# Kernel tuning notes

Measured on AMD Instinct MI355X. Metric: run time of the kernel, lower is better.

Reference implementation:

```python
import jax, jax.numpy as jnp
import numpy as np

MAX_LENGTH = 256
WIDTH = 4


def _attention_matrix(a, b):
    # a, b: (B, M, D) with M = max_length + width - 1
    # euclidean match score: 1 / (1 + ||a_i - b_j||_2)
    sq = (
        jnp.sum(a * a, axis=-1)[:, :, None]
        + jnp.sum(b * b, axis=-1)[:, None, :]
        - 2.0 * jnp.einsum('bid,bjd->bij', a, b)
    )
    dist = jnp.sqrt(jnp.maximum(sq, 0.0))
    return 1.0 / (1.0 + dist)  # (B, M, M)


def reference(x1, x2):
    # x1, x2: (B, 1, M, D), M = MAX_LENGTH + WIDTH - 1
    a = x1[:, 0]  # (B, M, D)
    b = x2[:, 0]
    A = _attention_matrix(a, b)  # (B, M, M), A[b,i,j] = score(a_i, b_j)
    # row_sum over dim i of A[:,:,k] weights x1 column k; col analogously for x2.
    w_a = jnp.sum(A, axis=1)  # (B, M): sum_i A[i, k]
    w_b = jnp.sum(A, axis=2)  # (B, M): sum_j A[k, j]
    y1 = w_a[:, :, None] * a  # (B, M, D)
    y2 = w_b[:, :, None] * b
    # sliding-window sum of width WIDTH: w[j] = sum_{k=j}^{j+WIDTH-1} y[k]
    w1 = sum(y1[:, d:d + MAX_LENGTH, :] for d in range(WIDTH))
    w2 = sum(y2[:, d:d + MAX_LENGTH, :] for d in range(WIDTH))
    return (w1[:, None], w2[:, None])  # (B, 1, MAX_LENGTH, D) each


def setup_inputs() -> dict:
    key = jax.random.key(0)
    k1, k2 = jax.random.split(key)
    B, M, D = 128, MAX_LENGTH + WIDTH - 1, 512
    x1 = jax.random.normal(k1, (B, 1, M, D), dtype=jnp.float32)
    x2 = jax.random.normal(k2, (B, 1, M, D), dtype=jnp.float32)
    return {"x1": x1, "x2": x2}
```

## Files before the change

### kernel.cpp

```cpp
#include <hip/hip_runtime.h>

#define BATCH 128
#define M 259
#define D 512
#define T 256
#define NM (BATCH * M)
#define OUTHALF (BATCH * T * D)

typedef __bf16 bf16;
typedef __bf16 bf16x4 __attribute__((ext_vector_type(4)));
typedef __bf16 bf16x8 __attribute__((ext_vector_type(8)));
typedef float f32x4 __attribute__((ext_vector_type(4)));


__global__ void k_norms(const float* __restrict__ x1, const float* __restrict__ x2,
                        float* __restrict__ ws) {
    int wave = blockIdx.x * 4 + (threadIdx.x >> 6);
    int lane = threadIdx.x & 63;
    if (wave >= NM) return;
    const float4* p1 = (const float4*)(x1 + (size_t)wave * D);
    const float4* p2 = (const float4*)(x2 + (size_t)wave * D);
    float s1 = 0.f, s2 = 0.f;
#pragma unroll
    for (int q = 0; q < 2; ++q) {
        float4 v = p1[lane + q * 64];
        s1 += v.x * v.x + v.y * v.y + v.z * v.z + v.w * v.w;
        float4 w = p2[lane + q * 64];
        s2 += w.x * w.x + w.y * w.y + w.z * w.z + w.w * w.w;
    }
#pragma unroll
    for (int off = 32; off > 0; off >>= 1) {
        s1 += __shfl_xor(s1, off);
        s2 += __shfl_xor(s2, off);
    }
    if (lane == 0) {
        ws[wave]          = s1;
        ws[NM + wave]     = s2;
        ws[2 * NM + wave] = 0.f;
        ws[3 * NM + wave] = 0.f;
    }
}

#define BT 96
#define BK 64
#define NTL 3

__launch_bounds__(256)
__global__ void k_pairs(const float* __restrict__ x1, const float* __restrict__ x2,
                        float* __restrict__ ws) {
    __shared__ __align__(16) bf16 As[2][BT * BK];
    __shared__ __align__(16) bf16 Bs[2][BT * BK];

    int s   = blockIdx.x;
    int bid = (s & 7) * 144 + (s >> 3);
    int b   = bid / 9;
    int ti  = (bid % 9) / 3;
    int tj  = bid % 3;
    int i0  = ti * BT, j0 = tj * BT;

    int t    = threadIdx.x;
    int lane = t & 63;
    int w    = t >> 6;
    int wm   = w >> 1, wn = w & 1;
    int iw   = i0 + wm * 48;
    int jw   = j0 + wn * 48;

    const float* Ab = x1 + (size_t)b * M * D;
    const float* Bb = x2 + (size_t)b * M * D;

    const float* pa[6];
    const float* pb[6];
    int c4 = (t & 15) * 4;
#pragma unroll
    for (int p = 0; p < 6; ++p) {
        int ra = min(i0 + p * 16 + (t >> 4), M - 1);
        int rb = min(j0 + p * 16 + (t >> 4), M - 1);
        pa[p] = Ab + (size_t)ra * D + c4;
        pb[p] = Bb + (size_t)rb * D + c4;
    }
    int wslot   = (t & 15) >> 1;
    int wwithin = (t & 1) * 4;
    int wr_off[6];
#pragma unroll
    for (int p = 0; p < 6; ++p) {
        int row = p * 16 + (t >> 4);
        wr_off[p] = row * BK + ((wslot ^ (row & 7)) << 3) + wwithin;
    }

    int a_off[3][2], b_off[3][2];
#pragma unroll
    for (int fm = 0; fm < 3; ++fm) {
        int rowa = wm * 48 + fm * 16 + (lane & 15);
        int rowb = wn * 48 + fm * 16 + (lane & 15);
#pragma unroll
        for (int kk = 0; kk < 2; ++kk) {
            int slot = kk * 4 + (lane >> 4);
            a_off[fm][kk] = rowa * BK + ((slot ^ (rowa & 7)) << 3);
            b_off[fm][kk] = rowb * BK + ((slot ^ (rowb & 7)) << 3);
        }
    }

    f32x4 acc[3][3];
#pragma unroll
    for (int fm = 0; fm < 3; ++fm)
#pragma unroll
        for (int fn = 0; fn < 3; ++fn) acc[fm][fn] = (f32x4)0.f;

    float4 va[6], vb[6];
#pragma unroll
    for (int p = 0; p < 6; ++p) {
        va[p] = *(const float4*)(pa[p]);
        vb[p] = *(const float4*)(pb[p]);
    }
#pragma unroll
    for (int p = 0; p < 6; ++p) {
        bf16x4 ca = { (bf16)va[p].x, (bf16)va[p].y, (bf16)va[p].z, (bf16)va[p].w };
        bf16x4 cb = { (bf16)vb[p].x, (bf16)vb[p].y, (bf16)vb[p].z, (bf16)vb[p].w };
        *(bf16x4*)&As[0][wr_off[p]] = ca;
        *(bf16x4*)&Bs[0][wr_off[p]] = cb;
    }
    __syncthreads();
#pragma unroll
    for (int p = 0; p < 6; ++p) {
        va[p] = *(const float4*)(pa[p] + BK);
        vb[p] = *(const float4*)(pb[p] + BK);
    }

    for (int k0 = 0; k0 < D; k0 += BK) {
        int cur = (k0 >> 6) & 1;
#pragma unroll
        for (int kk = 0; kk < 2; ++kk) {
            bf16x8 af[3], bfr[3];
#pragma unroll
            for (int fm = 0; fm < 3; ++fm) af[fm]  = *(const bf16x8*)&As[cur][a_off[fm][kk]];
#pragma unroll
            for (int fn = 0; fn < 3; ++fn) bfr[fn] = *(const bf16x8*)&Bs[cur][b_off[fn][kk]];
#pragma unroll
            for (int fm = 0; fm < 3; ++fm)
#pragma unroll
                for (int fn = 0; fn < 3; ++fn)
                    acc[fm][fn] = __builtin_amdgcn_mfma_f32_16x16x32_bf16(
                        af[fm], bfr[fn], acc[fm][fn], 0, 0, 0);
        }
        if (k0 + BK < D) {
#pragma unroll
            for (int p = 0; p < 6; ++p) {
                bf16x4 ca = { (bf16)va[p].x, (bf16)va[p].y, (bf16)va[p].z, (bf16)va[p].w };
                bf16x4 cb = { (bf16)vb[p].x, (bf16)vb[p].y, (bf16)vb[p].z, (bf16)vb[p].w };
                *(bf16x4*)&As[cur ^ 1][wr_off[p]] = ca;
                *(bf16x4*)&Bs[cur ^ 1][wr_off[p]] = cb;
            }
            __syncthreads();
            if (k0 + 2 * BK < D) {
#pragma unroll
                for (int p = 0; p < 6; ++p) {
                    va[p] = *(const float4*)(pa[p] + k0 + 2 * BK);
                    vb[p] = *(const float4*)(pb[p] + k0 + 2 * BK);
                }
            }
        }
    }

    int b_off_w = b * M;
    float na_[3][4], nb_[3];
#pragma unroll
    for (int fm = 0; fm < 3; ++fm)
#pragma unroll
        for (int r = 0; r < 4; ++r) {
            int i = iw + fm * 16 + (lane >> 4) * 4 + r;
            na_[fm][r] = (i < M) ? ws[b_off_w + i] : 0.f;
        }
#pragma unroll
    for (int fn = 0; fn < 3; ++fn) {
        int j = jw + fn * 16 + (lane & 15);
        nb_[fn] = (j < M) ? ws[NM + b_off_w + j] : 0.f;
    }

    float rs[3][4];
    float cs[3];
#pragma unroll
    for (int fm = 0; fm < 3; ++fm)
#pragma unroll
        for (int r = 0; r < 4; ++r) rs[fm][r] = 0.f;
#pragma unroll
    for (int fn = 0; fn < 3; ++fn) cs[fn] = 0.f;

#pragma unroll
    for (int fm = 0; fm < 3; ++fm) {
#pragma unroll
        for (int fn = 0; fn < 3; ++fn) {
#pragma unroll
            for (int r = 0; r < 4; ++r) {
                int i = iw + fm * 16 + (lane >> 4) * 4 + r;
                int j = jw + fn * 16 + (lane & 15);
                float av = 0.f;
                if (i < M && j < M) {
                    float sq   = na_[fm][r] + nb_[fn] - 2.f * acc[fm][fn][r];
                    float dist = sqrtf(fmaxf(sq, 0.f));
                    av = 1.f / (1.f + dist);
                }
                rs[fm][r] += av;
                cs[fn]    += av;
            }
        }
    }

#pragma unroll
    for (int fm = 0; fm < 3; ++fm)
#pragma unroll
        for (int r = 0; r < 4; ++r) {
            float v = rs[fm][r];
            v += __shfl_xor(v, 1); v += __shfl_xor(v, 2);
            v += __shfl_xor(v, 4); v += __shfl_xor(v, 8);
            int i = iw + fm * 16 + (lane >> 4) * 4 + r;
            if ((lane & 15) == 0 && i < M) atomicAdd(&ws[3 * NM + b_off_w + i], v);
        }
#pragma unroll
    for (int fn = 0; fn < 3; ++fn) {
        float v = cs[fn];
        v += __shfl_xor(v, 16); v += __shfl_xor(v, 32);
        int j = jw + fn * 16 + (lane & 15);
        if ((lane >> 4) == 0 && j < M) atomicAdd(&ws[2 * NM + b_off_w + j], v);
    }
}

__global__ void k_out(const float* __restrict__ x1, const float* __restrict__ x2,
                      const float* __restrict__ ws, float* __restrict__ out) {
    int bid   = blockIdx.x;
    int which = bid & 1;
    int tc    = (bid >> 1) & 7;
    int b     = bid >> 4;
    int d4    = threadIdx.x << 2;
    const float* src  = which ? x2 : x1;
    const float* wgt  = ws + (which ? 3 * NM : 2 * NM) + b * M;
    const float* rows = src + (size_t)b * M * D + d4;
    float* o = out + (size_t)which * OUTHALF + ((size_t)b * T + tc * 32) * D + d4;
    int t0 = tc * 32;
    float4 v0 = *(const float4*)(rows + (size_t)(t0 + 0) * D);
    float4 v1 = *(const float4*)(rows + (size_t)(t0 + 1) * D);
    float4 v2 = *(const float4*)(rows + (size_t)(t0 + 2) * D);
    float s0 = wgt[t0 + 0], s1 = wgt[t0 + 1], s2 = wgt[t0 + 2];
#pragma unroll 4
    for (int tt = 0; tt < 32; ++tt) {
        float4 v3 = *(const float4*)(rows + (size_t)(t0 + tt + 3) * D);
        float s3  = wgt[t0 + tt + 3];
        float4 r;
        r.x = s0 * v0.x + s1 * v1.x + s2 * v2.x + s3 * v3.x;
        r.y = s0 * v0.y + s1 * v1.y + s2 * v2.y + s3 * v3.y;
        r.z = s0 * v0.z + s1 * v1.z + s2 * v2.z + s3 * v3.z;
        r.w = s0 * v0.w + s1 * v1.w + s2 * v2.w + s3 * v3.w;
        *(float4*)(o + (size_t)tt * D) = r;
        v0 = v1; v1 = v2; v2 = v3;
        s0 = s1; s1 = s2; s2 = s3;
    }
}

extern "C" void kernel_launch(void* const* d_in, const int* in_sizes, int n_in,
                              void* d_out, int out_size, void* d_ws, size_t ws_size,
                              hipStream_t stream) {
    const float* x1 = (const float*)d_in[0];
    const float* x2 = (const float*)d_in[1];
    float* out = (float*)d_out;
    float* ws  = (float*)d_ws;

    k_norms<<<NM / 4, 256, 0, stream>>>(x1, x2, ws);
    k_pairs<<<BATCH * NTL * NTL, 256, 0, stream>>>(x1, x2, ws);
    k_out<<<BATCH * 16, 128, 0, stream>>>(x1, x2, ws, out);
}
```

Baseline: 117.3 us.

## Pre-convert inputs to bf16 and stream GEMM tiles via global_load_lds

The norm kernel now also writes bf16 copies of both inputs into workspace. The pair kernel then loads those copies straight into LDS with the global_load_lds builtin, using an XOR-swizzled layout, instead of loading fp32, converting and storing through registers. The intent is to halve GEMM global traffic and remove conversion work from the main loop, at the cost of an extra bf16 write and re-read pass. A single-buffered fp32 fallback runs when the workspace is too small.

After: 135.1 us. +15.2%, slower.

```diff
diff --git a/kernel.cpp b/kernel.cpp
--- a/kernel.cpp
+++ b/kernel.cpp
@@ -13,31 +13,42 @@
 typedef float f32x4 __attribute__((ext_vector_type(4)));
 
 
-__global__ void k_norms(const float* __restrict__ x1, const float* __restrict__ x2,
-                        float* __restrict__ ws) {
-    int wave = blockIdx.x * 4 + (threadIdx.x >> 6);
+__device__ __forceinline__ void gload16(const bf16* g, bf16* l) {
+    __builtin_amdgcn_global_load_lds(
+        (const __attribute__((address_space(1))) void*)g,
+        (__attribute__((address_space(3))) void*)l, 16, 0, 0);
+}
+
+__global__ void k_prep(const float* __restrict__ x1, const float* __restrict__ x2,
+                       float* __restrict__ ws, bf16* __restrict__ abf,
+                       bf16* __restrict__ bbf) {
+    int row  = blockIdx.x * 4 + (threadIdx.x >> 6);
     int lane = threadIdx.x & 63;
-    if (wave >= NM) return;
-    const float4* p1 = (const float4*)(x1 + (size_t)wave * D);
-    const float4* p2 = (const float4*)(x2 + (size_t)wave * D);
-    float s1 = 0.f, s2 = 0.f;
-#pragma unroll
-    for (int q = 0; q < 2; ++q) {
-        float4 v = p1[lane + q * 64];
-        s1 += v.x * v.x + v.y * v.y + v.z * v.z + v.w * v.w;
-        float4 w = p2[lane + q * 64];
-        s2 += w.x * w.x + w.y * w.y + w.z * w.z + w.w * w.w;
-    }
+    if (row >= NM) return;
+    const float4* p1 = (const float4*)(x1 + (size_t)row * D);
+    const float4* p2 = (const float4*)(x2 + (size_t)row * D);
+    float4 a0 = p1[lane], a1 = p1[lane + 64];
+    float4 b0 = p2[lane], b1 = p2[lane + 64];
+    float s1 = a0.x * a0.x + a0.y * a0.y + a0.z * a0.z + a0.w * a0.w
+             + a1.x * a1.x + a1.y * a1.y + a1.z * a1.z + a1.w * a1.w;
+    float s2 = b0.x * b0.x + b0.y * b0.y + b0.z * b0.z + b0.w * b0.w
+             + b1.x * b1.x + b1.y * b1.y + b1.z * b1.z + b1.w * b1.w;
+    bf16* ar = abf + (size_t)row * D;
+    bf16* br = bbf + (size_t)row * D;
+    *(bf16x4*)(ar + 4 * lane)       = bf16x4{ (bf16)a0.x, (bf16)a0.y, (bf16)a0.z, (bf16)a0.w };
+    *(bf16x4*)(ar + 256 + 4 * lane) = bf16x4{ (bf16)a1.x, (bf16)a1.y, (bf16)a1.z, (bf16)a1.w };
+    *(bf16x4*)(br + 4 * lane)       = bf16x4{ (bf16)b0.x, (bf16)b0.y, (bf16)b0.z, (bf16)b0.w };
+    *(bf16x4*)(br + 256 + 4 * lane) = bf16x4{ (bf16)b1.x, (bf16)b1.y, (bf16)b1.z, (bf16)b1.w };
 #pragma unroll
     for (int off = 32; off > 0; off >>= 1) {
         s1 += __shfl_xor(s1, off);
         s2 += __shfl_xor(s2, off);
     }
     if (lane == 0) {
-        ws[wave]          = s1;
-        ws[NM + wave]     = s2;
-        ws[2 * NM + wave] = 0.f;
-        ws[3 * NM + wave] = 0.f;
+        ws[row]          = s1;
+        ws[NM + row]     = s2;
+        ws[2 * NM + row] = 0.f;
+        ws[3 * NM + row] = 0.f;
     }
 }
 
@@ -46,8 +57,8 @@
 #define NTL 3
 
 __launch_bounds__(256)
-__global__ void k_pairs(const float* __restrict__ x1, const float* __restrict__ x2,
-                        float* __restrict__ ws) {
+__global__ void k_pairs_bf(const bf16* __restrict__ gA0, const bf16* __restrict__ gB0,
+                           float* __restrict__ ws) {
     __shared__ __align__(16) bf16 As[2][BT * BK];
     __shared__ __align__(16) bf16 Bs[2][BT * BK];
 
@@ -65,26 +76,17 @@
     int iw   = i0 + wm * 48;
     int jw   = j0 + wn * 48;
 
-    const float* Ab = x1 + (size_t)b * M * D;
-    const float* Bb = x2 + (size_t)b * M * D;
-
-    const float* pa[6];
-    const float* pb[6];
-    int c4 = (t & 15) * 4;
-#pragma unroll
-    for (int p = 0; p < 6; ++p) {
-        int ra = min(i0 + p * 16 + (t >> 4), M - 1);
-        int rb = min(j0 + p * 16 + (t >> 4), M - 1);
-        pa[p] = Ab + (size_t)ra * D + c4;
-        pb[p] = Bb + (size_t)rb * D + c4;
-    }
-    int wslot   = (t & 15) >> 1;
-    int wwithin = (t & 1) * 4;
-    int wr_off[6];
-#pragma unroll
-    for (int p = 0; p < 6; ++p) {
-        int row = p * 16 + (t >> 4);
-        wr_off[p] = row * BK + ((wslot ^ (row & 7)) << 3) + wwithin;
+    const bf16* gA = gA0 + (size_t)b * M * D;
+    const bf16* gB = gB0 + (size_t)b * M * D;
+
+    int wrow0 = w * 24;
+    int lrow  = lane >> 3;
+    int sl    = (lane & 7) ^ lrow;
+    int rA[3], rB[3];
+#pragma unroll
+    for (int i = 0; i < 3; ++i) {
+        rA[i] = min(i0 + wrow0 + 8 * i + lrow, M - 1);
+        rB[i] = min(j0 + wrow0 + 8 * i + lrow, M - 1);
     }
 
     int a_off[3][2], b_off[3][2];
@@ -106,28 +108,23 @@
 #pragma unroll
         for (int fn = 0; fn < 3; ++fn) acc[fm][fn] = (f32x4)0.f;
 
-    float4 va[6], vb[6];
-#pragma unroll
-    for (int p = 0; p < 6; ++p) {
-        va[p] = *(const float4*)(pa[p]);
-        vb[p] = *(const float4*)(pb[p]);
-    }
-#pragma unroll
-    for (int p = 0; p < 6; ++p) {
-        bf16x4 ca = { (bf16)va[p].x, (bf16)va[p].y, (bf16)va[p].z, (bf16)va[p].w };
-        bf16x4 cb = { (bf16)vb[p].x, (bf16)vb[p].y, (bf16)vb[p].z, (bf16)vb[p].w };
-        *(bf16x4*)&As[0][wr_off[p]] = ca;
-        *(bf16x4*)&Bs[0][wr_off[p]] = cb;
+#pragma unroll
+    for (int i = 0; i < 3; ++i) {
+        gload16(gA + (size_t)rA[i] * D + sl * 8, &As[0][(wrow0 + 8 * i) * BK]);
+        gload16(gB + (size_t)rB[i] * D + sl * 8, &Bs[0][(wrow0 + 8 * i) * BK]);
     }
     __syncthreads();
-#pragma unroll
-    for (int p = 0; p < 6; ++p) {
-        va[p] = *(const float4*)(pa[p] + BK);
-        vb[p] = *(const float4*)(pb[p] + BK);
-    }
-
-    for (int k0 = 0; k0 < D; k0 += BK) {
-        int cur = (k0 >> 6) & 1;
+
+    for (int t8 = 0; t8 < 8; ++t8) {
+        int cur = t8 & 1;
+        if (t8 + 1 < 8) {
+            int k0 = (t8 + 1) * BK;
+#pragma unroll
+            for (int i = 0; i < 3; ++i) {
+                gload16(gA + (size_t)rA[i] * D + k0 + sl * 8, &As[cur ^ 1][(wrow0 + 8 * i) * BK]);
+                gload16(gB + (size_t)rB[i] * D + k0 + sl * 8, &Bs[cur ^ 1][(wrow0 + 8 * i) * BK]);
+            }
+        }
 #pragma unroll
         for (int kk = 0; kk < 2; ++kk) {
             bf16x8 af[3], bfr[3];
@@ -142,23 +139,7 @@
                     acc[fm][fn] = __builtin_amdgcn_mfma_f32_16x16x32_bf16(
                         af[fm], bfr[fn], acc[fm][fn], 0, 0, 0);
         }
-        if (k0 + BK < D) {
-#pragma unroll
-            for (int p = 0; p < 6; ++p) {
-                bf16x4 ca = { (bf16)va[p].x, (bf16)va[p].y, (bf16)va[p].z, (bf16)va[p].w };
-                bf16x4 cb = { (bf16)vb[p].x, (bf16)vb[p].y, (bf16)vb[p].z, (bf16)vb[p].w };
-                *(bf16x4*)&As[cur ^ 1][wr_off[p]] = ca;
-                *(bf16x4*)&Bs[cur ^ 1][wr_off[p]] = cb;
-            }
-            __syncthreads();
-            if (k0 + 2 * BK < D) {
-#pragma unroll
-                for (int p = 0; p < 6; ++p) {
-                    va[p] = *(const float4*)(pa[p] + k0 + 2 * BK);
-                    vb[p] = *(const float4*)(pb[p] + k0 + 2 * BK);
-                }
-            }
-        }
+        __syncthreads();
     }
 
     int b_off_w = b * M;
@@ -176,8 +157,7 @@
         nb_[fn] = (j < M) ? ws[NM + b_off_w + j] : 0.f;
     }
 
-    float rs[3][4];
-    float cs[3];
+    float rs[3][4], cs[3];
 #pragma unroll
     for (int fm = 0; fm < 3; ++fm)
 #pragma unroll
@@ -205,6 +185,167 @@
         }
     }
 
+#pragma unroll
+    for (int fm = 0; fm < 3; ++fm)
+#pragma unroll
+        for (int r = 0; r < 4; ++r) {
+            float v = rs[fm][r];
+            v += __shfl_xor(v, 1); v += __shfl_xor(v, 2);
+            v += __shfl_xor(v, 4); v += __shfl_xor(v, 8);
+            int i = iw + fm * 16 + (lane >> 4) * 4 + r;
+            if ((lane & 15) == 0 && i < M) atomicAdd(&ws[3 * NM + b_off_w + i], v);
+        }
+#pragma unroll
+    for (int fn = 0; fn < 3; ++fn) {
+        float v = cs[fn];
+        v += __shfl_xor(v, 16); v += __shfl_xor(v, 32);
+        int j = jw + fn * 16 + (lane & 15);
+        if ((lane >> 4) == 0 && j < M) atomicAdd(&ws[2 * NM + b_off_w + j], v);
+    }
+}
+
+__global__ void k_norms(const float* __restrict__ x1, const float* __restrict__ x2,
+                        float* __restrict__ ws) {
+    int row  = blockIdx.x * 4 + (threadIdx.x >> 6);
+    int lane = threadIdx.x & 63;
+    if (row >= NM) return;
+    const float4* p1 = (const float4*)(x1 + (size_t)row * D);
+    const float4* p2 = (const float4*)(x2 + (size_t)row * D);
+    float s1 = 0.f, s2 = 0.f;
+#pragma unroll
+    for (int q = 0; q < 2; ++q) {
+        float4 v = p1[lane + q * 64];
+        s1 += v.x * v.x + v.y * v.y + v.z * v.z + v.w * v.w;
+        float4 u = p2[lane + q * 64];
+        s2 += u.x * u.x + u.y * u.y + u.z * u.z + u.w * u.w;
+    }
+#pragma unroll
+    for (int off = 32; off > 0; off >>= 1) {
+        s1 += __shfl_xor(s1, off);
+        s2 += __shfl_xor(s2, off);
+    }
+    if (lane == 0) {
+        ws[row] = s1; ws[NM + row] = s2;
+        ws[2 * NM + row] = 0.f; ws[3 * NM + row] = 0.f;
+    }
+}
+
+__launch_bounds__(256)
+__global__ void k_pairs_fb(const float* __restrict__ x1, const float* __restrict__ x2,
+                           float* __restrict__ ws) {
+    __shared__ __align__(16) bf16 As[BT * BK];
+    __shared__ __align__(16) bf16 Bs[BT * BK];
+    int s   = blockIdx.x;
+    int bid = (s & 7) * 144 + (s >> 3);
+    int b   = bid / 9;
+    int ti  = (bid % 9) / 3;
+    int tj  = bid % 3;
+    int i0  = ti * BT, j0 = tj * BT;
+    int t    = threadIdx.x;
+    int lane = t & 63;
+    int w    = t >> 6;
+    int wm   = w >> 1, wn = w & 1;
+    int iw   = i0 + wm * 48, jw = j0 + wn * 48;
+    const float* Ab = x1 + (size_t)b * M * D;
+    const float* Bb = x2 + (size_t)b * M * D;
+    const float* pa[6]; const float* pb[6];
+    int c4 = (t & 15) * 4;
+#pragma unroll
+    for (int p = 0; p < 6; ++p) {
+        int ra = min(i0 + p * 16 + (t >> 4), M - 1);
+        int rb = min(j0 + p * 16 + (t >> 4), M - 1);
+        pa[p] = Ab + (size_t)ra * D + c4;
+        pb[p] = Bb + (size_t)rb * D + c4;
+    }
+    int wslot = (t & 15) >> 1, wwithin = (t & 1) * 4;
+    int wr_off[6];
+#pragma unroll
+    for (int p = 0; p < 6; ++p) {
+        int row = p * 16 + (t >> 4);
+        wr_off[p] = row * BK + ((wslot ^ (row & 7)) << 3) + wwithin;
+    }
+    int a_off[3][2], b_off[3][2];
+#pragma unroll
+    for (int fm = 0; fm < 3; ++fm) {
+        int rowa = wm * 48 + fm * 16 + (lane & 15);
+        int rowb = wn * 48 + fm * 16 + (lane & 15);
+#pragma unroll
+        for (int kk = 0; kk < 2; ++kk) {
+            int slot = kk * 4 + (lane >> 4);
+            a_off[fm][kk] = rowa * BK + ((slot ^ (rowa & 7)) << 3);
+            b_off[fm][kk] = rowb * BK + ((slot ^ (rowb & 7)) << 3);
+        }
+    }
+    f32x4 acc[3][3];
+#pragma unroll
+    for (int fm = 0; fm < 3; ++fm)
+#pragma unroll
+        for (int fn = 0; fn < 3; ++fn) acc[fm][fn] = (f32x4)0.f;
+    for (int k0 = 0; k0 < D; k0 += BK) {
+        float4 va[6], vb[6];
+#pragma unroll
+        for (int p = 0; p < 6; ++p) {
+            va[p] = *(const float4*)(pa[p] + k0);
+            vb[p] = *(const float4*)(pb[p] + k0);
+        }
+        __syncthreads();
+#pragma unroll
+        for (int p = 0; p < 6; ++p) {
+            *(bf16x4*)&As[wr_off[p]] = bf16x4{ (bf16)va[p].x, (bf16)va[p].y, (bf16)va[p].z, (bf16)va[p].w };
+            *(bf16x4*)&Bs[wr_off[p]] = bf16x4{ (bf16)vb[p].x, (bf16)vb[p].y, (bf16)vb[p].z, (bf16)vb[p].w };
+        }
+        __syncthreads();
+#pragma unroll
+        for (int kk = 0; kk < 2; ++kk) {
+            bf16x8 af[3], bfr[3];
+#pragma unroll
+            for (int fm = 0; fm < 3; ++fm) af[fm]  = *(const bf16x8*)&As[a_off[fm][kk]];
+#pragma unroll
+            for (int fn = 0; fn < 3; ++fn) bfr[fn] = *(const bf16x8*)&Bs[b_off[fn][kk]];
+#pragma unroll
+            for (int fm = 0; fm < 3; ++fm)
+#pragma unroll
+                for (int fn = 0; fn < 3; ++fn)
+                    acc[fm][fn] = __builtin_amdgcn_mfma_f32_16x16x32_bf16(
+                        af[fm], bfr[fn], acc[fm][fn], 0, 0, 0);
+        }
+    }
+    int b_off_w = b * M;
+    float na_[3][4], nb_[3];
+#pragma unroll
+    for (int fm = 0; fm < 3; ++fm)
+#pragma unroll
+        for (int r = 0; r < 4; ++r) {
+            int i = iw + fm * 16 + (lane >> 4) * 4 + r;
+            na_[fm][r] = (i < M) ? ws[b_off_w + i] : 0.f;
+        }
+#pragma unroll
+    for (int fn = 0; fn < 3; ++fn) {
+        int j = jw + fn * 16 + (lane & 15);
+        nb_[fn] = (j < M) ? ws[NM + b_off_w + j] : 0.f;
+    }
+    float rs[3][4], cs[3];
+#pragma unroll
+    for (int fm = 0; fm < 3; ++fm)
+#pragma unroll
+        for (int r = 0; r < 4; ++r) rs[fm][r] = 0.f;
+#pragma unroll
+    for (int fn = 0; fn < 3; ++fn) cs[fn] = 0.f;
+#pragma unroll
+    for (int fm = 0; fm < 3; ++fm)
+#pragma unroll
+        for (int fn = 0; fn < 3; ++fn)
+#pragma unroll
+            for (int r = 0; r < 4; ++r) {
+                int i = iw + fm * 16 + (lane >> 4) * 4 + r;
+                int j = jw + fn * 16 + (lane & 15);
+                float av = 0.f;
+                if (i < M && j < M) {
+                    float sq = na_[fm][r] + nb_[fn] - 2.f * acc[fm][fn][r];
+                    av = 1.f / (1.f + sqrtf(fmaxf(sq, 0.f)));
+                }
+                rs[fm][r] += av; cs[fn] += av;
+            }
 #pragma unroll
     for (int fm = 0; fm < 3; ++fm)
 #pragma unroll
@@ -263,7 +404,15 @@
     float* out = (float*)d_out;
     float* ws  = (float*)d_ws;
 
-    k_norms<<<NM / 4, 256, 0, stream>>>(x1, x2, ws);
-    k_pairs<<<BATCH * NTL * NTL, 256, 0, stream>>>(x1, x2, ws);
+    size_t need = sizeof(float) * 4 * (size_t)NM + sizeof(bf16) * 2 * (size_t)NM * D;
+    if (ws_size >= need) {
+        bf16* abf = (bf16*)(ws + 4 * (size_t)NM);
+        bf16* bbf = abf + (size_t)NM * D;
+        k_prep<<<NM / 4, 256, 0, stream>>>(x1, x2, ws, abf, bbf);
+        k_pairs_bf<<<BATCH * NTL * NTL, 256, 0, stream>>>(abf, bbf, ws);
+    } else {
+        k_norms<<<NM / 4, 256, 0, stream>>>(x1, x2, ws);
+        k_pairs_fb<<<BATCH * NTL * NTL, 256, 0, stream>>>(x1, x2, ws);
+    }
     k_out<<<BATCH * 16, 128, 0, stream>>>(x1, x2, ws, out);
 }
```

## Enlarge pair tile to 144x144 with 9 waves and single-buffered LDS

Applied to the files above, without the earlier changes.

Switches the Gram-matrix kernel from 3x3 tiles of 96 with 4 waves to 2x2 tiles of 144 with 9 waves per block (576 threads). The goal is to cut redundant global loads and fp32-to-bf16 conversions by reusing each loaded row across more of the output tile. It also drops LDS double buffering and register prefetch in favour of a simple load, sync, store, sync loop. That adds two barriers per k-step and exposes global load latency, and the grid shrinks to 512 blocks. The 2x144 tiling also covers rows past M=259, which wastes some compute.

Measured after the change: 119.3 us. About the same (+1.7%).

```diff
diff --git a/kernel.cpp b/kernel.cpp
--- a/kernel.cpp
+++ b/kernel.cpp
@@ -15,18 +15,18 @@
 
 __global__ void k_norms(const float* __restrict__ x1, const float* __restrict__ x2,
                         float* __restrict__ ws) {
-    int wave = blockIdx.x * 4 + (threadIdx.x >> 6);
+    int row  = blockIdx.x * 4 + (threadIdx.x >> 6);
     int lane = threadIdx.x & 63;
-    if (wave >= NM) return;
-    const float4* p1 = (const float4*)(x1 + (size_t)wave * D);
-    const float4* p2 = (const float4*)(x2 + (size_t)wave * D);
+    if (row >= NM) return;
+    const float4* p1 = (const float4*)(x1 + (size_t)row * D);
+    const float4* p2 = (const float4*)(x2 + (size_t)row * D);
     float s1 = 0.f, s2 = 0.f;
 #pragma unroll
     for (int q = 0; q < 2; ++q) {
         float4 v = p1[lane + q * 64];
         s1 += v.x * v.x + v.y * v.y + v.z * v.z + v.w * v.w;
-        float4 w = p2[lane + q * 64];
-        s2 += w.x * w.x + w.y * w.y + w.z * w.z + w.w * w.w;
+        float4 u = p2[lane + q * 64];
+        s2 += u.x * u.x + u.y * u.y + u.z * u.z + u.w * u.w;
     }
 #pragma unroll
     for (int off = 32; off > 0; off >>= 1) {
@@ -34,56 +34,55 @@
         s2 += __shfl_xor(s2, off);
     }
     if (lane == 0) {
-        ws[wave]          = s1;
-        ws[NM + wave]     = s2;
-        ws[2 * NM + wave] = 0.f;
-        ws[3 * NM + wave] = 0.f;
-    }
-}
-
-#define BT 96
+        ws[row]          = s1;
+        ws[NM + row]     = s2;
+        ws[2 * NM + row] = 0.f;
+        ws[3 * NM + row] = 0.f;
+    }
+}
+
+#define BT 144
 #define BK 64
-#define NTL 3
-
-__launch_bounds__(256)
+
 __global__ void k_pairs(const float* __restrict__ x1, const float* __restrict__ x2,
                         float* __restrict__ ws) {
-    __shared__ __align__(16) bf16 As[2][BT * BK];
-    __shared__ __align__(16) bf16 Bs[2][BT * BK];
+    __shared__ __align__(16) bf16 As[BT * BK];
+    __shared__ __align__(16) bf16 Bs[BT * BK];
 
     int s   = blockIdx.x;
-    int bid = (s & 7) * 144 + (s >> 3);
-    int b   = bid / 9;
-    int ti  = (bid % 9) / 3;
-    int tj  = bid % 3;
+    int bid = (s & 7) * 64 + (s >> 3);
+    int b   = bid >> 2;
+    int ti  = (bid >> 1) & 1;
+    int tj  = bid & 1;
     int i0  = ti * BT, j0 = tj * BT;
 
     int t    = threadIdx.x;
     int lane = t & 63;
-    int w    = t >> 6;
-    int wm   = w >> 1, wn = w & 1;
+    int w    = t / 64;
+    int wm   = w / 3, wn = w % 3;
     int iw   = i0 + wm * 48;
     int jw   = j0 + wn * 48;
 
     const float* Ab = x1 + (size_t)b * M * D;
     const float* Bb = x2 + (size_t)b * M * D;
 
-    const float* pa[6];
-    const float* pb[6];
+    const float* pa[4];
+    const float* pb[4];
     int c4 = (t & 15) * 4;
 #pragma unroll
-    for (int p = 0; p < 6; ++p) {
-        int ra = min(i0 + p * 16 + (t >> 4), M - 1);
-        int rb = min(j0 + p * 16 + (t >> 4), M - 1);
+    for (int p = 0; p < 4; ++p) {
+        int row = p * 36 + (t >> 4);
+        int ra = min(i0 + row, M - 1);
+        int rb = min(j0 + row, M - 1);
         pa[p] = Ab + (size_t)ra * D + c4;
         pb[p] = Bb + (size_t)rb * D + c4;
     }
     int wslot   = (t & 15) >> 1;
     int wwithin = (t & 1) * 4;
-    int wr_off[6];
-#pragma unroll
-    for (int p = 0; p < 6; ++p) {
-        int row = p * 16 + (t >> 4);
+    int wr_off[4];
+#pragma unroll
+    for (int p = 0; p < 4; ++p) {
+        int row = p * 36 + (t >> 4);
         wr_off[p] = row * BK + ((wslot ^ (row & 7)) << 3) + wwithin;
     }
 
@@ -106,35 +105,27 @@
 #pragma unroll
         for (int fn = 0; fn < 3; ++fn) acc[fm][fn] = (f32x4)0.f;
 
-    float4 va[6], vb[6];
-#pragma unroll
-    for (int p = 0; p < 6; ++p) {
-        va[p] = *(const float4*)(pa[p]);
-        vb[p] = *(const float4*)(pb[p]);
-    }
-#pragma unroll
-    for (int p = 0; p < 6; ++p) {
-        bf16x4 ca = { (bf16)va[p].x, (bf16)va[p].y, (bf16)va[p].z, (bf16)va[p].w };
-        bf16x4 cb = { (bf16)vb[p].x, (bf16)vb[p].y, (bf16)vb[p].z, (bf16)vb[p].w };
-        *(bf16x4*)&As[0][wr_off[p]] = ca;
-        *(bf16x4*)&Bs[0][wr_off[p]] = cb;
-    }
-    __syncthreads();
-#pragma unroll
-    for (int p = 0; p < 6; ++p) {
-        va[p] = *(const float4*)(pa[p] + BK);
-        vb[p] = *(const float4*)(pb[p] + BK);
-    }
-
     for (int k0 = 0; k0 < D; k0 += BK) {
-        int cur = (k0 >> 6) & 1;
+        float4 va[4], vb[4];
+#pragma unroll
+        for (int p = 0; p < 4; ++p) {
+            va[p] = *(const float4*)(pa[p] + k0);
+            vb[p] = *(const float4*)(pb[p] + k0);
+        }
+        __syncthreads();
+#pragma unroll
+        for (int p = 0; p < 4; ++p) {
+            *(bf16x4*)&As[wr_off[p]] = bf16x4{ (bf16)va[p].x, (bf16)va[p].y, (bf16)va[p].z, (bf16)va[p].w };
+            *(bf16x4*)&Bs[wr_off[p]] = bf16x4{ (bf16)vb[p].x, (bf16)vb[p].y, (bf16)vb[p].z, (bf16)vb[p].w };
+        }
+        __syncthreads();
 #pragma unroll
         for (int kk = 0; kk < 2; ++kk) {
             bf16x8 af[3], bfr[3];
 #pragma unroll
-            for (int fm = 0; fm < 3; ++fm) af[fm]  = *(const bf16x8*)&As[cur][a_off[fm][kk]];
-#pragma unroll
-            for (int fn = 0; fn < 3; ++fn) bfr[fn] = *(const bf16x8*)&Bs[cur][b_off[fn][kk]];
+            for (int fm = 0; fm < 3; ++fm) af[fm]  = *(const bf16x8*)&As[a_off[fm][kk]];
+#pragma unroll
+            for (int fn = 0; fn < 3; ++fn) bfr[fn] = *(const bf16x8*)&Bs[b_off[fn][kk]];
 #pragma unroll
             for (int fm = 0; fm < 3; ++fm)
 #pragma unroll
@@ -142,23 +133,6 @@
                     acc[fm][fn] = __builtin_amdgcn_mfma_f32_16x16x32_bf16(
                         af[fm], bfr[fn], acc[fm][fn], 0, 0, 0);
         }
-        if (k0 + BK < D) {
-#pragma unroll
-            for (int p = 0; p < 6; ++p) {
-                bf16x4 ca = { (bf16)va[p].x, (bf16)va[p].y, (bf16)va[p].z, (bf16)va[p].w };
-                bf16x4 cb = { (bf16)vb[p].x, (bf16)vb[p].y, (bf16)vb[p].z, (bf16)vb[p].w };
-                *(bf16x4*)&As[cur ^ 1][wr_off[p]] = ca;
-                *(bf16x4*)&Bs[cur ^ 1][wr_off[p]] = cb;
-            }
-            __syncthreads();
-            if (k0 + 2 * BK < D) {
-#pragma unroll
-                for (int p = 0; p < 6; ++p) {
-                    va[p] = *(const float4*)(pa[p] + k0 + 2 * BK);
-                    vb[p] = *(const float4*)(pb[p] + k0 + 2 * BK);
-                }
-            }
-        }
     }
 
     int b_off_w = b * M;
@@ -176,8 +150,7 @@
         nb_[fn] = (j < M) ? ws[NM + b_off_w + j] : 0.f;
     }
 
-    float rs[3][4];
-    float cs[3];
+    float rs[3][4], cs[3];
 #pragma unroll
     for (int fm = 0; fm < 3; ++fm)
 #pragma unroll
@@ -264,6 +237,6 @@
     float* ws  = (float*)d_ws;
 
     k_norms<<<NM / 4, 256, 0, stream>>>(x1, x2, ws);
-    k_pairs<<<BATCH * NTL * NTL, 256, 0, stream>>>(x1, x2, ws);
+    k_pairs<<<512, 576, 0, stream>>>(x1, x2, ws);
     k_out<<<BATCH * 16, 128, 0, stream>>>(x1, x2, ws, out);
 }
```
